# Kernel tuning notes

Hardware: AMD Instinct MI355X
Metric: run time of the kernel (lower is better)

Reference implementation:

```python
import jax, jax.numpy as jnp
import numpy as np

B, N, R, NF, NH = 2, 2048, 16384, 128, 3
PSTEP = 3


def _lin(x, w, b):
    return x @ w + b


def _mlp2(x, w0, b0, w1, b1):
    return jax.nn.relu(_lin(jax.nn.relu(_lin(x, w0, b0)), w1, b1))


def setup_inputs() -> dict:
    key = jax.random.key(0)
    ks = jax.random.split(key, 16)

    def w(k, i, o):
        return (jax.random.normal(k, (i, o), dtype=jnp.float32) / np.float32(np.sqrt(i)))

    a_cur = jax.random.uniform(ks[0], (B, N), dtype=jnp.float32)
    s_cur = jax.random.normal(ks[1], (B, N, 3), dtype=jnp.float32)
    s_delta = jax.random.normal(ks[2], (B, NH, N, 3), dtype=jnp.float32)
    # Rr/Rs: dense one-hot receiver/sender matrices (B, rel_num, N)
    Rr = jax.nn.one_hot(jax.random.randint(ks[3], (B, R), 0, N), N, dtype=jnp.float32)
    Rs = jax.nn.one_hot(jax.random.randint(ks[4], (B, R), 0, N), N, dtype=jnp.float32)
    edge_attrs = (jax.random.uniform(ks[5], (B, R, 1)) > 0.5).astype(jnp.float32)
    z = lambda n: jnp.zeros((n,), dtype=jnp.float32)
    return {
        "a_cur": a_cur, "s_cur": s_cur, "s_delta": s_delta,
        "Rr": Rr, "Rs": Rs, "edge_attrs": edge_attrs,
        "pe_w0": w(ks[6], 3 * NH + 1, NF), "pe_b0": z(NF),
        "pe_w1": w(ks[7], NF, NF), "pe_b1": z(NF),
        "re_w0": w(ks[8], 6, NF), "re_b0": z(NF),
        "re_w1": w(ks[9], NF, NF), "re_b1": z(NF),
        "re_w2": w(ks[10], NF, NF), "re_b2": z(NF),
        "rp_w": w(ks[11], 3 * NF, NF), "rp_b": z(NF),
        "pp_w": w(ks[12], 2 * NF, NF), "pp_b": z(NF),
        "pr_w0": w(ks[13], NF, NF), "pr_b0": z(NF),
        "pr_w1": w(ks[14], NF, 3), "pr_b1": z(3),
    }


def reference(a_cur, s_cur, s_delta, Rr, Rs, edge_attrs,
              pe_w0, pe_b0, pe_w1, pe_b1,
              re_w0, re_b0, re_w1, re_b1, re_w2, re_b2,
              rp_w, rp_b, pp_w, pp_b,
              pr_w0, pr_b0, pr_w1, pr_b1):
    b, nh, n, _ = s_delta.shape
    # (B, n_history, N, 3) -> (B, N, 3*n_history)
    s_delta_flat = jnp.transpose(s_delta, (0, 2, 1, 3)).reshape(b, n, -1)
    a_r = jnp.einsum('brn,bn->br', Rr, a_cur)[..., None]
    a_s = jnp.einsum('brn,bn->br', Rs, a_cur)[..., None]
    s_r = jnp.einsum('brn,bnd->brd', Rr, s_cur)
    s_s = jnp.einsum('brn,bnd->brd', Rs, s_cur)

    particle_encode = _mlp2(jnp.concatenate([s_delta_flat, a_cur[..., None]], -1),
                            pe_w0, pe_b0, pe_w1, pe_b1)
    rel_in = jnp.concatenate([a_r, a_s, s_r - s_s, edge_attrs], -1)
    relation_encode = jax.nn.relu(_lin(
        jax.nn.relu(_lin(jax.nn.relu(_lin(rel_in, re_w0, re_b0)), re_w1, re_b1)),
        re_w2, re_b2))

    effect = particle_encode
    for _ in range(PSTEP):
        e_r = jnp.einsum('brn,bnf->brf', Rr, effect)
        e_s = jnp.einsum('brn,bnf->brf', Rs, effect)
        e_rel = jax.nn.relu(_lin(jnp.concatenate([relation_encode, e_r, e_s], -1), rp_w, rp_b))
        agg = jnp.einsum('brn,brf->bnf', Rr, e_rel)  # Rr^T aggregation
        effect = jax.nn.relu(
            _lin(jnp.concatenate([particle_encode, agg], -1), pp_w, pp_b) + effect)

    pred = _lin(jax.nn.relu(_lin(effect, pr_w0, pr_b0)), pr_w1, pr_b1)
    return pred + s_cur
```

## Files before the change

kernel.cpp:

```cpp
#include <hip/hip_runtime.h>
#include <hip/hip_bf16.h>
#include <stdint.h>

#define B_ 2
#define N_ 2048
#define R_ 16384
#define NF_ 128
#define NH_ 3
#define PSTEP_ 3
#define EDGES (B_ * R_)
#define NODES (B_ * N_)
#define MAXDEG 64
#define PREP_EXB0 1024

typedef _Float16 f16;
typedef _Float16 f16x4 __attribute__((ext_vector_type(4)));
typedef float f32x4 __attribute__((ext_vector_type(4)));

struct GemmLds { f16 Ah[128 * 128], Al[128 * 128], Bh[128 * 128], Bl[128 * 128]; };
struct VecLds {
  float wbuf[64][NF_];
  float xt[NF_][20];
  float ht[NF_][20];
  float w0s[10][NF_];
  float b0s[NF_], b1s[NF_];
  float xs[16][10];
  float w1s[NF_][4];
};
union MainLds { GemmLds g; VecLds v; };

__device__ __forceinline__ void gl16(const f16* g, f16* l) {
  typedef const __attribute__((address_space(1))) uint32_t* gas_t;
  typedef __attribute__((address_space(3))) uint32_t* las_t;
  __builtin_amdgcn_global_load_lds((gas_t)(const void*)g, (las_t)(void*)l, 16, 0, 0);
}

__device__ __forceinline__ void mfma_block(const f16* Ah, const f16* Al,
                                           const f16* Bh, const f16* Bl,
                                           f32x4 (&acc)[8][2], int lane, int w) {
  const int l16 = lane & 15, l4 = lane >> 4;
  #pragma unroll 1
  for (int kk = 0; kk < 8; ++kk) {
    const int c16 = kk * 2 + (l4 >> 1);
    const int sub = (l4 & 1) * 4;
    f16x4 bh[2], bl[2];
    #pragma unroll
    for (int nf = 0; nf < 2; ++nf) {
      const int n = w * 32 + nf * 16 + l16;
      const int off = n * 128 + ((c16 ^ (n & 7)) * 8) + sub;
      bh[nf] = *(const f16x4*)&Bh[off];
      bl[nf] = *(const f16x4*)&Bl[off];
    }
    #pragma unroll
    for (int m = 0; m < 8; ++m) {
      const int r = m * 16 + l16;
      const int off = r * 128 + ((c16 ^ (r & 7)) * 8) + sub;
      const f16x4 ah = *(const f16x4*)&Ah[off];
      const f16x4 al = *(const f16x4*)&Al[off];
      #pragma unroll
      for (int nf = 0; nf < 2; ++nf) {
        acc[m][nf] = __builtin_amdgcn_mfma_f32_16x16x16f16(ah, bh[nf], acc[m][nf], 0, 0, 0);
        acc[m][nf] = __builtin_amdgcn_mfma_f32_16x16x16f16(ah, bl[nf], acc[m][nf], 0, 0, 0);
        acc[m][nf] = __builtin_amdgcn_mfma_f32_16x16x16f16(al, bh[nf], acc[m][nf], 0, 0, 0);
      }
    }
  }
}

__device__ __forceinline__ void frags_to_lds(f32x4 (&acc)[8][2], f16* Ah, f16* Al,
                                             int lane, int w) {
  const int l16 = lane & 15, l4 = lane >> 4;
  #pragma unroll
  for (int m = 0; m < 8; ++m)
    #pragma unroll
    for (int nf = 0; nf < 2; ++nf)
      #pragma unroll
      for (int i = 0; i < 4; ++i) {
        const float v = fmaxf(acc[m][nf][i], 0.f);
        const int row = m * 16 + l4 * 4 + i;
        const int col = w * 32 + nf * 16 + l16;
        const int off = row * 128 + (((col >> 3) ^ (row & 7)) * 8) + (col & 7);
        const f16 h = (f16)v;
        Ah[off] = h; Al[off] = (f16)(v - (float)h);
      }
}

__global__ __launch_bounds__(256) void k_prep(
    const float* __restrict__ Rr, const float* __restrict__ Rs,
    const float* __restrict__ rp_w, const float* __restrict__ re_w1,
    const float* __restrict__ re_w2,
    int* __restrict__ recv, int* __restrict__ send,
    f16* __restrict__ rpT_h, f16* __restrict__ rpT_l,
    f16* __restrict__ re1T_h, f16* __restrict__ re1T_l,
    f16* __restrict__ re2T_h, f16* __restrict__ re2T_l,
    int* __restrict__ counts) {
  const int bid = blockIdx.x, t = threadIdx.x;
  if (bid < 16) {
    counts[bid * 256 + t] = 0;
  } else if (bid < 336) {
    const int i = (bid - 16) * 256 + t;
    const int S1 = 384 * 128, S2 = S1 + 128 * 128, S3 = S2 + 128 * 128;
    if (i < S1) {
      const int k = i >> 7, n = i & 127;
      const float v = rp_w[i];
      const f16 h = (f16)v;
      rpT_h[n * 384 + k] = h; rpT_l[n * 384 + k] = (f16)(v - (float)h);
    } else if (i < S2) {
      const int j = i - S1, k = j >> 7, n = j & 127;
      const float v = re_w1[j];
      const f16 h = (f16)v;
      re1T_h[n * 128 + k] = h; re1T_l[n * 128 + k] = (f16)(v - (float)h);
    } else if (i < S3) {
      const int j = i - S2, k = j >> 7, n = j & 127;
      const float v = re_w2[j];
      const f16 h = (f16)v;
      re2T_h[n * 128 + k] = h; re2T_l[n * 128 + k] = (f16)(v - (float)h);
    }
  } else if (bid >= PREP_EXB0) {
    const int wid = (bid - PREP_EXB0) * 4 + (t >> 6);
    const int lane = t & 63;
    const bool isR = wid < EDGES;
    const int row = isR ? wid : wid - EDGES;
    const float4* p = reinterpret_cast<const float4*>((isR ? Rr : Rs) + (size_t)row * N_);
    int found = 0;
    #pragma unroll 1
    for (int it = 0; it < N_ / 256; ++it) {
      const float4 v = p[it * 64 + lane];
      const int base = (it * 64 + lane) * 4;
      bool hit = false;
      if (v.x != 0.f) { found = base;     hit = true; }
      if (v.y != 0.f) { found = base + 1; hit = true; }
      if (v.z != 0.f) { found = base + 2; hit = true; }
      if (v.w != 0.f) { found = base + 3; hit = true; }
      if (__any(hit)) break;
    }
    #pragma unroll
    for (int off = 32; off > 0; off >>= 1)
      found = max(found, __shfl_down(found, off, 64));
    if (lane == 0) (isR ? recv : send)[row] = found;
  }
}

__global__ __launch_bounds__(256, 1) void k_pre(
    const float* __restrict__ a_cur, const float* __restrict__ s_cur,
    const float* __restrict__ s_delta, const float* __restrict__ ea,
    const int* __restrict__ recv, const int* __restrict__ send,
    const float* __restrict__ pe_w0, const float* __restrict__ pe_b0,
    const float* __restrict__ pe_w1, const float* __restrict__ pe_b1,
    const float* __restrict__ re_w0, const float* __restrict__ re_b0,
    const float* __restrict__ re_b1, const float* __restrict__ re_b2,
    const f16* __restrict__ re1T_h, const f16* __restrict__ re1T_l,
    const f16* __restrict__ re2T_h, const f16* __restrict__ re2T_l,
    float* __restrict__ pe, f16* __restrict__ pe_h, f16* __restrict__ pe_l,
    f16* __restrict__ rel_h, f16* __restrict__ rel_l,
    int* __restrict__ counts, int* __restrict__ bucket) {
  __shared__ MainLds u;
  __shared__ float xt6[6][128];
  __shared__ float w0s6[6][128];
  __shared__ float sb0[128];

  const int bid = blockIdx.x, t = threadIdx.x;
  const int lane = t & 63, w = t >> 6;
  const int l16 = lane & 15, l4 = lane >> 4;
  const int f = t & 127, g = t >> 7;

  {
    const int e = bid * 256 + t;
    if (e < EDGES) {
      const int gnode = (e >> 14) * N_ + recv[e];
      const int pos = atomicAdd(&counts[gnode], 1);
      if (pos < MAXDEG) bucket[gnode * MAXDEG + pos] = e;
    }
  }

  auto stageB = [&](const f16* gh, const f16* gl) {
    #pragma unroll
    for (int rb = 0; rb < 32; rb += 4) {
      const int r0w = w * 32 + rb;
      const int row = r0w + l4;
      const int sc = (l16 ^ (row & 7)) * 8;
      gl16(gh + (size_t)row * 128 + sc, &u.g.Bh[r0w * 128]);
      gl16(gl + (size_t)row * 128 + sc, &u.g.Bl[r0w * 128]);
    }
  };

  {
    const int r0 = bid * 16;
    for (int i = t; i < 10 * NF_; i += 256) u.v.w0s[i >> 7][i & 127] = pe_w0[i];
    if (t < NF_) { u.v.b0s[t] = pe_b0[t]; u.v.b1s[t] = pe_b1[t]; }
    for (int i = t; i < 160; i += 256) {
      const int r = i / 10, k = i % 10;
      const int gr = r0 + r, b = gr >> 11, n = gr & (N_ - 1);
      u.v.xs[r][k] = (k < 9)
          ? s_delta[(((size_t)b * NH_ + (k / 3)) * N_ + n) * 3 + (k % 3)]
          : a_cur[gr];
    }
    __syncthreads();
    for (int r = g * 8; r < g * 8 + 8; ++r) {
      float a1 = u.v.b0s[f];
      #pragma unroll
      for (int k = 0; k < 10; ++k) a1 = fmaf(u.v.xs[r][k], u.v.w0s[k][f], a1);
      u.v.ht[f][r] = fmaxf(a1, 0.f);
    }
    float acc[8];
    #pragma unroll
    for (int i = 0; i < 8; ++i) acc[i] = u.v.b1s[f];
    for (int h = 0; h < 2; ++h) {
      __syncthreads();
      for (int i = t; i < 64 * NF_; i += 256) u.v.wbuf[i >> 7][i & 127] = pe_w1[h * 64 * NF_ + i];
      __syncthreads();
      for (int k = 0; k < 64; ++k) {
        const float wv = u.v.wbuf[k][f];
        #pragma unroll
        for (int i = 0; i < 2; ++i) {
          const float4 x4 = *reinterpret_cast<const float4*>(&u.v.ht[h * 64 + k][g * 8 + i * 4]);
          acc[i*4+0] = fmaf(x4.x, wv, acc[i*4+0]);
          acc[i*4+1] = fmaf(x4.y, wv, acc[i*4+1]);
          acc[i*4+2] = fmaf(x4.z, wv, acc[i*4+2]);
          acc[i*4+3] = fmaf(x4.w, wv, acc[i*4+3]);
        }
      }
    }
    #pragma unroll
    for (int i = 0; i < 8; ++i) {
      const size_t idx = (size_t)(r0 + g * 8 + i) * NF_ + f;
      const float v = fmaxf(acc[i], 0.f);
      pe[idx] = v;
      const f16 h = (f16)v;
      pe_h[idx] = h; pe_l[idx] = (f16)(v - (float)h);
    }
  }
  __syncthreads();

  {
    const int e0 = bid * 128;
    if (t < 128) {
      const int ge = e0 + t, b = ge >> 14;
      const int rc = recv[ge], sd = send[ge];
      xt6[0][t] = a_cur[(b << 11) + rc];
      xt6[1][t] = a_cur[(b << 11) + sd];
      #pragma unroll
      for (int d = 0; d < 3; ++d)
        xt6[2 + d][t] = s_cur[(size_t)((b << 11) + rc) * 3 + d]
                      - s_cur[(size_t)((b << 11) + sd) * 3 + d];
      xt6[5][t] = ea[ge];
    }
    stageB(re1T_h, re1T_l);
    for (int i = t; i < 6 * 128; i += 256) w0s6[i >> 7][i & 127] = re_w0[i];
    if (t < 128) sb0[t] = re_b0[t];
    __syncthreads();
    {
      float wreg[6];
      #pragma unroll
      for (int k = 0; k < 6; ++k) wreg[k] = w0s6[k][f];
      const float b0v = sb0[f];
      for (int r = g * 64; r < g * 64 + 64; ++r) {
        float a1 = b0v;
        #pragma unroll
        for (int k = 0; k < 6; ++k) a1 = fmaf(xt6[k][r], wreg[k], a1);
        a1 = fmaxf(a1, 0.f);
        const int off = r * 128 + ((((f >> 3)) ^ (r & 7)) * 8) + (f & 7);
        const f16 h = (f16)a1;
        u.g.Ah[off] = h; u.g.Al[off] = (f16)(a1 - (float)h);
      }
    }
    __syncthreads();
    f32x4 acc[8][2];
    {
      const float bv0 = re_b1[w * 32 + l16], bv1 = re_b1[w * 32 + 16 + l16];
      #pragma unroll
      for (int m = 0; m < 8; ++m) {
        acc[m][0] = (f32x4){bv0, bv0, bv0, bv0};
        acc[m][1] = (f32x4){bv1, bv1, bv1, bv1};
      }
    }
    mfma_block(u.g.Ah, u.g.Al, u.g.Bh, u.g.Bl, acc, lane, w);
    __syncthreads();
    frags_to_lds(acc, u.g.Ah, u.g.Al, lane, w);
    stageB(re2T_h, re2T_l);
    {
      const float bv0 = re_b2[w * 32 + l16], bv1 = re_b2[w * 32 + 16 + l16];
      #pragma unroll
      for (int m = 0; m < 8; ++m) {
        acc[m][0] = (f32x4){bv0, bv0, bv0, bv0};
        acc[m][1] = (f32x4){bv1, bv1, bv1, bv1};
      }
    }
    __syncthreads();
    mfma_block(u.g.Ah, u.g.Al, u.g.Bh, u.g.Bl, acc, lane, w);
    __syncthreads();
    frags_to_lds(acc, u.g.Ah, u.g.Al, lane, w);
    __syncthreads();
    {
      const int row = t >> 1, hf = t & 1;
      const float4* sA = (const float4*)&u.g.Ah[row * 128 + hf * 64];
      const float4* sL = (const float4*)&u.g.Al[row * 128 + hf * 64];
      float4* dA = (float4*)&rel_h[(size_t)(e0 + row) * 128 + hf * 64];
      float4* dL = (float4*)&rel_l[(size_t)(e0 + row) * 128 + hf * 64];
      #pragma unroll
      for (int j = 0; j < 8; ++j) { dA[j] = sA[j]; dL[j] = sL[j]; }
    }
  }
}

__global__ __launch_bounds__(256, 1) void k_erel(
    const f16* __restrict__ rel_h, const f16* __restrict__ rel_l,
    const f16* __restrict__ src_h, const f16* __restrict__ src_l,
    const int* __restrict__ recv, const int* __restrict__ send,
    const f16* __restrict__ rpT_h, const f16* __restrict__ rpT_l,
    const float* __restrict__ rp_b, float* __restrict__ e_rel) {
  __shared__ GemmLds u;
  __shared__ int eidx0[128], eidx1[128];
  const int bid = blockIdx.x, t = threadIdx.x;
  const int lane = t & 63, w = t >> 6;
  const int l16 = lane & 15, l4 = lane >> 4;
  const int e0 = bid * 128;
  const int b = bid >> 7;
  if (t < 128) eidx0[t] = recv[e0 + t];
  else         eidx1[t - 128] = send[e0 + t - 128];
  f32x4 acc[8][2];
  {
    const float bv0 = rp_b[w * 32 + l16], bv1 = rp_b[w * 32 + 16 + l16];
    #pragma unroll
    for (int m = 0; m < 8; ++m) {
      acc[m][0] = (f32x4){bv0, bv0, bv0, bv0};
      acc[m][1] = (f32x4){bv1, bv1, bv1, bv1};
    }
  }
  #pragma unroll 1
  for (int ch = 0; ch < 3; ++ch) {
    __syncthreads();
    #pragma unroll
    for (int rb = 0; rb < 32; rb += 4) {
      const int r0w = w * 32 + rb;
      const int row = r0w + l4;
      const int ge = e0 + row;
      if (ch == 0) {
        gl16(rel_h + (size_t)ge * 128 + l16 * 8, &u.Ah[r0w * 128]);
        gl16(rel_l + (size_t)ge * 128 + l16 * 8, &u.Al[r0w * 128]);
      } else {
        const int node = (ch == 1) ? eidx0[row] : eidx1[row];
        const size_t ao = ((size_t)(b << 11) + node) * 128 + ((l16 ^ (row & 7)) * 8);
        gl16(src_h + ao, &u.Ah[r0w * 128]);
        gl16(src_l + ao, &u.Al[r0w * 128]);
      }
      const int sc = (l16 ^ (row & 7)) * 8;
      gl16(rpT_h + (size_t)row * 384 + ch * 128 + sc, &u.Bh[r0w * 128]);
      gl16(rpT_l + (size_t)row * 384 + ch * 128 + sc, &u.Bl[r0w * 128]);
    }
    __syncthreads();
    mfma_block(u.Ah, u.Al, u.Bh, u.Bl, acc, lane, w);
  }
  #pragma unroll
  for (int m = 0; m < 8; ++m)
    #pragma unroll
    for (int nf = 0; nf < 2; ++nf)
      #pragma unroll
      for (int i = 0; i < 4; ++i) {
        const float v = fmaxf(acc[m][nf][i], 0.f);
        const int row = e0 + m * 16 + l4 * 4 + i;
        const int col = w * 32 + nf * 16 + l16;
        e_rel[(size_t)row * NF_ + col] = v;
      }
}

__global__ __launch_bounds__(256) void k_update(
    const float* __restrict__ pe, const float* __restrict__ e_rel,
    const int* __restrict__ counts, const int* __restrict__ bucket,
    const float* __restrict__ src_f,
    const float* __restrict__ pp_w, const float* __restrict__ pp_b,
    float* __restrict__ dst_f, f16* __restrict__ dst_h, f16* __restrict__ dst_l,
    const float* __restrict__ s_cur,
    const float* __restrict__ pr_w0, const float* __restrict__ pr_b0,
    const float* __restrict__ pr_w1, const float* __restrict__ pr_b1,
    float* __restrict__ out, int final_step) {
  __shared__ alignas(16) float wbuf[64][NF_];
  __shared__ alignas(16) float xt[NF_][20];
  __shared__ alignas(16) float ht[NF_][20];
  __shared__ float w1s[NF_][4];
  const int t = threadIdx.x, f = t & 127, g = t >> 7;
  const int r0 = blockIdx.x * 16;
  float acc[8];
  {
    const float bias = pp_b[f];
    #pragma unroll
    for (int i = 0; i < 8; ++i) acc[i] = bias;
  }
  for (int c = 0; c < 2; ++c) {
    __syncthreads();
    {
      const int e = t >> 4, k0 = (t & 15) * 8;
      float s[8];
      if (c == 0) {
        const float* srcp = pe + (size_t)(r0 + e) * NF_ + k0;
        const float4 v0 = *reinterpret_cast<const float4*>(srcp);
        const float4 v1 = *reinterpret_cast<const float4*>(srcp + 4);
        s[0]=v0.x; s[1]=v0.y; s[2]=v0.z; s[3]=v0.w;
        s[4]=v1.x; s[5]=v1.y; s[6]=v1.z; s[7]=v1.w;
      } else {
        #pragma unroll
        for (int i = 0; i < 8; ++i) s[i] = 0.f;
        const int gnode = r0 + e;
        const int cnt = min(counts[gnode], MAXDEG);
        for (int i = 0; i < cnt; ++i) {
          const int ed = bucket[gnode * MAXDEG + i];
          const float4 v0 = *reinterpret_cast<const float4*>(&e_rel[(size_t)ed * NF_ + k0]);
          const float4 v1 = *reinterpret_cast<const float4*>(&e_rel[(size_t)ed * NF_ + k0 + 4]);
          s[0]+=v0.x; s[1]+=v0.y; s[2]+=v0.z; s[3]+=v0.w;
          s[4]+=v1.x; s[5]+=v1.y; s[6]+=v1.z; s[7]+=v1.w;
        }
      }
      #pragma unroll
      for (int i = 0; i < 8; ++i) xt[k0 + i][e] = s[i];
    }
    #pragma unroll 1
    for (int h = 0; h < 2; ++h) {
      __syncthreads();
      for (int i = t; i < 64 * NF_; i += 256)
        wbuf[i >> 7][i & 127] = pp_w[(size_t)(c * NF_ + h * 64) * NF_ + i];
      __syncthreads();
      for (int k = 0; k < 64; ++k) {
        const float wv = wbuf[k][f];
        const int ka = h * 64 + k;
        #pragma unroll
        for (int i = 0; i < 2; ++i) {
          const float4 x4 = *reinterpret_cast<const float4*>(&xt[ka][g * 8 + i * 4]);
          acc[i*4+0] = fmaf(x4.x, wv, acc[i*4+0]);
          acc[i*4+1] = fmaf(x4.y, wv, acc[i*4+1]);
          acc[i*4+2] = fmaf(x4.z, wv, acc[i*4+2]);
          acc[i*4+3] = fmaf(x4.w, wv, acc[i*4+3]);
        }
      }
    }
  }
  if (!final_step) {
    #pragma unroll
    for (int i = 0; i < 8; ++i) {
      const size_t idx = (size_t)(r0 + g * 8 + i) * NF_ + f;
      const float v = fmaxf(acc[i] + src_f[idx], 0.f);
      dst_f[idx] = v;
      const f16 h = (f16)v;
      dst_h[idx] = h; dst_l[idx] = (f16)(v - (float)h);
    }
    return;
  }
  __syncthreads();
  #pragma unroll
  for (int i = 0; i < 8; ++i) {
    const size_t idx = (size_t)(r0 + g * 8 + i) * NF_ + f;
    xt[f][g * 8 + i] = fmaxf(acc[i] + src_f[idx], 0.f);
  }
  for (int i = t; i < NF_ * 3; i += 256) w1s[i / 3][i % 3] = pr_w1[i];
  {
    const float bias = pr_b0[f];
    #pragma unroll
    for (int i = 0; i < 8; ++i) acc[i] = bias;
  }
  for (int h = 0; h < 2; ++h) {
    __syncthreads();
    for (int i = t; i < 64 * NF_; i += 256) wbuf[i >> 7][i & 127] = pr_w0[h * 64 * NF_ + i];
    __syncthreads();
    for (int k = 0; k < 64; ++k) {
      const float wv = wbuf[k][f];
      const int ka = h * 64 + k;
      #pragma unroll
      for (int i = 0; i < 2; ++i) {
        const float4 x4 = *reinterpret_cast<const float4*>(&xt[ka][g * 8 + i * 4]);
        acc[i*4+0] = fmaf(x4.x, wv, acc[i*4+0]);
        acc[i*4+1] = fmaf(x4.y, wv, acc[i*4+1]);
        acc[i*4+2] = fmaf(x4.z, wv, acc[i*4+2]);
        acc[i*4+3] = fmaf(x4.w, wv, acc[i*4+3]);
      }
    }
  }
  #pragma unroll
  for (int i = 0; i < 8; ++i) ht[f][g * 8 + i] = fmaxf(acc[i], 0.f);
  __syncthreads();
  if (t < 48) {
    const int r = t / 3, d = t % 3;
    float a2 = pr_b1[d];
    for (int k = 0; k < NF_; ++k) a2 = fmaf(ht[k][r], w1s[k][d], a2);
    const int gr = r0 + r;
    out[(size_t)gr * 3 + d] = a2 + s_cur[(size_t)gr * 3 + d];
  }
}

extern "C" void kernel_launch(void* const* d_in, const int* in_sizes, int n_in,
                              void* d_out, int out_size, void* d_ws, size_t ws_size,
                              hipStream_t stream) {
  (void)in_sizes; (void)n_in; (void)out_size; (void)ws_size;
  const float* a_cur   = (const float*)d_in[0];
  const float* s_cur   = (const float*)d_in[1];
  const float* s_delta = (const float*)d_in[2];
  const float* Rr      = (const float*)d_in[3];
  const float* Rs      = (const float*)d_in[4];
  const float* ea      = (const float*)d_in[5];
  const float* pe_w0 = (const float*)d_in[6];
  const float* pe_b0 = (const float*)d_in[7];
  const float* pe_w1 = (const float*)d_in[8];
  const float* pe_b1 = (const float*)d_in[9];
  const float* re_w0 = (const float*)d_in[10];
  const float* re_b0 = (const float*)d_in[11];
  const float* re_w1 = (const float*)d_in[12];
  const float* re_b1 = (const float*)d_in[13];
  const float* re_w2 = (const float*)d_in[14];
  const float* re_b2 = (const float*)d_in[15];
  const float* rp_w  = (const float*)d_in[16];
  const float* rp_b  = (const float*)d_in[17];
  const float* pp_w  = (const float*)d_in[18];
  const float* pp_b  = (const float*)d_in[19];
  const float* pr_w0 = (const float*)d_in[20];
  const float* pr_b0 = (const float*)d_in[21];
  const float* pr_w1 = (const float*)d_in[22];
  const float* pr_b1 = (const float*)d_in[23];
  float* out = (float*)d_out;

  uint8_t* wp = (uint8_t*)d_ws;
  auto alloc = [&](size_t bytes) {
    void* p = (void*)wp;
    wp += (bytes + 255) & ~(size_t)255;
    return p;
  };
  int* recv   = (int*)alloc(EDGES * 4);
  int* send   = (int*)alloc(EDGES * 4);
  int* counts = (int*)alloc(NODES * 4);
  int* bucket = (int*)alloc((size_t)NODES * MAXDEG * 4);
  float* pe   = (float*)alloc((size_t)NODES * NF_ * 4);
  f16* pe_h   = (f16*)alloc((size_t)NODES * NF_ * 2);
  f16* pe_l   = (f16*)alloc((size_t)NODES * NF_ * 2);
  float* effA = (float*)alloc((size_t)NODES * NF_ * 4);
  f16* effA_h = (f16*)alloc((size_t)NODES * NF_ * 2);
  f16* effA_l = (f16*)alloc((size_t)NODES * NF_ * 2);
  float* effB = (float*)alloc((size_t)NODES * NF_ * 4);
  f16* effB_h = (f16*)alloc((size_t)NODES * NF_ * 2);
  f16* effB_l = (f16*)alloc((size_t)NODES * NF_ * 2);
  float* e_rel = (float*)alloc((size_t)EDGES * NF_ * 4);
  f16* rel_h  = (f16*)alloc((size_t)EDGES * NF_ * 2);
  f16* rel_l  = (f16*)alloc((size_t)EDGES * NF_ * 2);
  f16* rpT_h  = (f16*)alloc(128 * 384 * 2);
  f16* rpT_l  = (f16*)alloc(128 * 384 * 2);
  f16* re1T_h = (f16*)alloc(128 * 128 * 2);
  f16* re1T_l = (f16*)alloc(128 * 128 * 2);
  f16* re2T_h = (f16*)alloc(128 * 128 * 2);
  f16* re2T_l = (f16*)alloc(128 * 128 * 2);

  k_prep<<<PREP_EXB0 + (2 * EDGES) / 4, 256, 0, stream>>>(
      Rr, Rs, rp_w, re_w1, re_w2, recv, send,
      rpT_h, rpT_l, re1T_h, re1T_l, re2T_h, re2T_l, counts);

  k_pre<<<256, 256, 0, stream>>>(
      a_cur, s_cur, s_delta, ea, recv, send,
      pe_w0, pe_b0, pe_w1, pe_b1, re_w0, re_b0, re_b1, re_b2,
      re1T_h, re1T_l, re2T_h, re2T_l,
      pe, pe_h, pe_l, rel_h, rel_l, counts, bucket);

  const float* esrc = pe;
  const f16* esrc_h = pe_h;
  const f16* esrc_l = pe_l;
  for (int s = 0; s < PSTEP_; ++s) {
    float* dst_f = (s == 1) ? effB   : effA;
    f16*  dst_h  = (s == 1) ? effB_h : effA_h;
    f16*  dst_l  = (s == 1) ? effB_l : effA_l;
    k_erel<<<EDGES / 128, 256, 0, stream>>>(rel_h, rel_l, esrc_h, esrc_l,
                                            recv, send, rpT_h, rpT_l, rp_b, e_rel);
    k_update<<<NODES / 16, 256, 0, stream>>>(
        pe, e_rel, counts, bucket, esrc, pp_w, pp_b, dst_f, dst_h, dst_l,
        s_cur, pr_w0, pr_b0, pr_w1, pr_b1, out, (s == PSTEP_ - 1) ? 1 : 0);
    esrc = dst_f; esrc_h = dst_h; esrc_l = dst_l;
  }
}
```

Before: 692.5 us.

## Drop split-f16 hi/lo emulation, use single f16 MFMA and smaller edge tiles

```diff
diff --git a/kernel.cpp b/kernel.cpp
--- a/kernel.cpp
+++ b/kernel.cpp
@@ -17,7 +17,8 @@
 typedef _Float16 f16x4 __attribute__((ext_vector_type(4)));
 typedef float f32x4 __attribute__((ext_vector_type(4)));
 
-struct GemmLds { f16 Ah[128 * 128], Al[128 * 128], Bh[128 * 128], Bl[128 * 128]; };
+struct GemmLds128 { f16 Ah[128 * 128], Bh[128 * 128]; };
+struct GemmLds64  { f16 Ah[64 * 128],  Bh[128 * 128]; };
 struct VecLds {
   float wbuf[64][NF_];
   float xt[NF_][20];
@@ -27,7 +28,7 @@
   float xs[16][10];
   float w1s[NF_][4];
 };
-union MainLds { GemmLds g; VecLds v; };
+union PreLds { GemmLds128 g; VecLds v; };
 
 __device__ __forceinline__ void gl16(const f16* g, f16* l) {
   typedef const __attribute__((address_space(1))) uint32_t* gas_t;
@@ -35,39 +36,32 @@
   __builtin_amdgcn_global_load_lds((gas_t)(const void*)g, (las_t)(void*)l, 16, 0, 0);
 }
 
-__device__ __forceinline__ void mfma_block(const f16* Ah, const f16* Al,
-                                           const f16* Bh, const f16* Bl,
-                                           f32x4 (&acc)[8][2], int lane, int w) {
+template<int MM>
+__device__ __forceinline__ void mfma_blockT(const f16* Ah, const f16* Bh,
+                                            f32x4 (&acc)[MM][2], int lane, int w) {
   const int l16 = lane & 15, l4 = lane >> 4;
   #pragma unroll 1
   for (int kk = 0; kk < 8; ++kk) {
     const int c16 = kk * 2 + (l4 >> 1);
     const int sub = (l4 & 1) * 4;
-    f16x4 bh[2], bl[2];
+    f16x4 bh[2];
     #pragma unroll
     for (int nf = 0; nf < 2; ++nf) {
       const int n = w * 32 + nf * 16 + l16;
-      const int off = n * 128 + ((c16 ^ (n & 7)) * 8) + sub;
-      bh[nf] = *(const f16x4*)&Bh[off];
-      bl[nf] = *(const f16x4*)&Bl[off];
-    }
-    #pragma unroll
-    for (int m = 0; m < 8; ++m) {
+      bh[nf] = *(const f16x4*)&Bh[n * 128 + ((c16 ^ (n & 7)) * 8) + sub];
+    }
+    #pragma unroll
+    for (int m = 0; m < MM; ++m) {
       const int r = m * 16 + l16;
-      const int off = r * 128 + ((c16 ^ (r & 7)) * 8) + sub;
-      const f16x4 ah = *(const f16x4*)&Ah[off];
-      const f16x4 al = *(const f16x4*)&Al[off];
-      #pragma unroll
-      for (int nf = 0; nf < 2; ++nf) {
+      const f16x4 ah = *(const f16x4*)&Ah[r * 128 + ((c16 ^ (r & 7)) * 8) + sub];
+      #pragma unroll
+      for (int nf = 0; nf < 2; ++nf)
         acc[m][nf] = __builtin_amdgcn_mfma_f32_16x16x16f16(ah, bh[nf], acc[m][nf], 0, 0, 0);
-        acc[m][nf] = __builtin_amdgcn_mfma_f32_16x16x16f16(ah, bl[nf], acc[m][nf], 0, 0, 0);
-        acc[m][nf] = __builtin_amdgcn_mfma_f32_16x16x16f16(al, bh[nf], acc[m][nf], 0, 0, 0);
-      }
-    }
-  }
-}
-
-__device__ __forceinline__ void frags_to_lds(f32x4 (&acc)[8][2], f16* Ah, f16* Al,
+    }
+  }
+}
+
+__device__ __forceinline__ void frags_to_lds(f32x4 (&acc)[8][2], f16* Ah,
                                              int lane, int w) {
   const int l16 = lane & 15, l4 = lane >> 4;
   #pragma unroll
@@ -79,9 +73,7 @@
         const float v = fmaxf(acc[m][nf][i], 0.f);
         const int row = m * 16 + l4 * 4 + i;
         const int col = w * 32 + nf * 16 + l16;
-        const int off = row * 128 + (((col >> 3) ^ (row & 7)) * 8) + (col & 7);
-        const f16 h = (f16)v;
-        Ah[off] = h; Al[off] = (f16)(v - (float)h);
+        Ah[row * 128 + (((col >> 3) ^ (row & 7)) * 8) + (col & 7)] = (f16)v;
       }
 }
 
@@ -90,9 +82,7 @@
     const float* __restrict__ rp_w, const float* __restrict__ re_w1,
     const float* __restrict__ re_w2,
     int* __restrict__ recv, int* __restrict__ send,
-    f16* __restrict__ rpT_h, f16* __restrict__ rpT_l,
-    f16* __restrict__ re1T_h, f16* __restrict__ re1T_l,
-    f16* __restrict__ re2T_h, f16* __restrict__ re2T_l,
+    f16* __restrict__ rpT_h, f16* __restrict__ re1T_h, f16* __restrict__ re2T_h,
     int* __restrict__ counts) {
   const int bid = blockIdx.x, t = threadIdx.x;
   if (bid < 16) {
@@ -102,19 +92,13 @@
     const int S1 = 384 * 128, S2 = S1 + 128 * 128, S3 = S2 + 128 * 128;
     if (i < S1) {
       const int k = i >> 7, n = i & 127;
-      const float v = rp_w[i];
-      const f16 h = (f16)v;
-      rpT_h[n * 384 + k] = h; rpT_l[n * 384 + k] = (f16)(v - (float)h);
+      rpT_h[n * 384 + k] = (f16)rp_w[i];
     } else if (i < S2) {
       const int j = i - S1, k = j >> 7, n = j & 127;
-      const float v = re_w1[j];
-      const f16 h = (f16)v;
-      re1T_h[n * 128 + k] = h; re1T_l[n * 128 + k] = (f16)(v - (float)h);
+      re1T_h[n * 128 + k] = (f16)re_w1[j];
     } else if (i < S3) {
       const int j = i - S2, k = j >> 7, n = j & 127;
-      const float v = re_w2[j];
-      const f16 h = (f16)v;
-      re2T_h[n * 128 + k] = h; re2T_l[n * 128 + k] = (f16)(v - (float)h);
+      re2T_h[n * 128 + k] = (f16)re_w2[j];
     }
   } else if (bid >= PREP_EXB0) {
     const int wid = (bid - PREP_EXB0) * 4 + (t >> 6);
@@ -141,7 +125,7 @@
   }
 }
 
-__global__ __launch_bounds__(256, 1) void k_pre(
+__global__ __launch_bounds__(256, 2) void k_pre(
     const float* __restrict__ a_cur, const float* __restrict__ s_cur,
     const float* __restrict__ s_delta, const float* __restrict__ ea,
     const int* __restrict__ recv, const int* __restrict__ send,
@@ -149,12 +133,11 @@
     const float* __restrict__ pe_w1, const float* __restrict__ pe_b1,
     const float* __restrict__ re_w0, const float* __restrict__ re_b0,
     const float* __restrict__ re_b1, const float* __restrict__ re_b2,
-    const f16* __restrict__ re1T_h, const f16* __restrict__ re1T_l,
-    const f16* __restrict__ re2T_h, const f16* __restrict__ re2T_l,
-    float* __restrict__ pe, f16* __restrict__ pe_h, f16* __restrict__ pe_l,
-    f16* __restrict__ rel_h, f16* __restrict__ rel_l,
+    const f16* __restrict__ re1T_h, const f16* __restrict__ re2T_h,
+    float* __restrict__ pe, f16* __restrict__ pe_h,
+    f16* __restrict__ rel_h,
     int* __restrict__ counts, int* __restrict__ bucket) {
-  __shared__ MainLds u;
+  __shared__ PreLds u;
   __shared__ float xt6[6][128];
   __shared__ float w0s6[6][128];
   __shared__ float sb0[128];
@@ -164,6 +147,9 @@
   const int l16 = lane & 15, l4 = lane >> 4;
   const int f = t & 127, g = t >> 7;
 
+  {
+    const int e = bid * 128 + t;
+  }
   {
     const int e = bid * 256 + t;
     if (e < EDGES) {
@@ -173,14 +159,13 @@
     }
   }
 
-  auto stageB = [&](const f16* gh, const f16* gl) {
+  auto stageB = [&](const f16* gh) {
     #pragma unroll
     for (int rb = 0; rb < 32; rb += 4) {
       const int r0w = w * 32 + rb;
       const int row = r0w + l4;
       const int sc = (l16 ^ (row & 7)) * 8;
       gl16(gh + (size_t)row * 128 + sc, &u.g.Bh[r0w * 128]);
-      gl16(gl + (size_t)row * 128 + sc, &u.g.Bl[r0w * 128]);
     }
   };
 
@@ -190,9 +175,9 @@
     if (t < NF_) { u.v.b0s[t] = pe_b0[t]; u.v.b1s[t] = pe_b1[t]; }
     for (int i = t; i < 160; i += 256) {
       const int r = i / 10, k = i % 10;
-      const int gr = r0 + r, b = gr >> 11, n = gr & (N_ - 1);
+      const int gr = r0 + r, bb = gr >> 11, n = gr & (N_ - 1);
       u.v.xs[r][k] = (k < 9)
-          ? s_delta[(((size_t)b * NH_ + (k / 3)) * N_ + n) * 3 + (k % 3)]
+          ? s_delta[(((size_t)bb * NH_ + (k / 3)) * N_ + n) * 3 + (k % 3)]
           : a_cur[gr];
     }
     __syncthreads();
@@ -226,8 +211,7 @@
       const size_t idx = (size_t)(r0 + g * 8 + i) * NF_ + f;
       const float v = fmaxf(acc[i], 0.f);
       pe[idx] = v;
-      const f16 h = (f16)v;
-      pe_h[idx] = h; pe_l[idx] = (f16)(v - (float)h);
+      pe_h[idx] = (f16)v;
     }
   }
   __syncthreads();
@@ -235,17 +219,17 @@
   {
     const int e0 = bid * 128;
     if (t < 128) {
-      const int ge = e0 + t, b = ge >> 14;
+      const int ge = e0 + t, bb = ge >> 14;
       const int rc = recv[ge], sd = send[ge];
-      xt6[0][t] = a_cur[(b << 11) + rc];
-      xt6[1][t] = a_cur[(b << 11) + sd];
+      xt6[0][t] = a_cur[(bb << 11) + rc];
+      xt6[1][t] = a_cur[(bb << 11) + sd];
       #pragma unroll
       for (int d = 0; d < 3; ++d)
-        xt6[2 + d][t] = s_cur[(size_t)((b << 11) + rc) * 3 + d]
-                      - s_cur[(size_t)((b << 11) + sd) * 3 + d];
+        xt6[2 + d][t] = s_cur[(size_t)((bb << 11) + rc) * 3 + d]
+                      - s_cur[(size_t)((bb << 11) + sd) * 3 + d];
       xt6[5][t] = ea[ge];
     }
-    stageB(re1T_h, re1T_l);
+    stageB(re1T_h);
     for (int i = t; i < 6 * 128; i += 256) w0s6[i >> 7][i & 127] = re_w0[i];
     if (t < 128) sb0[t] = re_b0[t];
     __syncthreads();
@@ -259,9 +243,7 @@
         #pragma unroll
         for (int k = 0; k < 6; ++k) a1 = fmaf(xt6[k][r], wreg[k], a1);
         a1 = fmaxf(a1, 0.f);
-        const int off = r * 128 + ((((f >> 3)) ^ (r & 7)) * 8) + (f & 7);
-        const f16 h = (f16)a1;
-        u.g.Ah[off] = h; u.g.Al[off] = (f16)(a1 - (float)h);
+        u.g.Ah[r * 128 + ((((f >> 3)) ^ (r & 7)) * 8) + (f & 7)] = (f16)a1;
       }
     }
     __syncthreads();
@@ -274,10 +256,10 @@
         acc[m][1] = (f32x4){bv1, bv1, bv1, bv1};
       }
     }
-    mfma_block(u.g.Ah, u.g.Al, u.g.Bh, u.g.Bl, acc, lane, w);
-    __syncthreads();
-    frags_to_lds(acc, u.g.Ah, u.g.Al, lane, w);
-    stageB(re2T_h, re2T_l);
+    mfma_blockT<8>(u.g.Ah, u.g.Bh, acc, lane, w);
+    __syncthreads();
+    frags_to_lds(acc, u.g.Ah, lane, w);
+    stageB(re2T_h);
     {
       const float bv0 = re_b2[w * 32 + l16], bv1 = re_b2[w * 32 + 16 + l16];
       #pragma unroll
@@ -287,42 +269,39 @@
       }
     }
     __syncthreads();
-    mfma_block(u.g.Ah, u.g.Al, u.g.Bh, u.g.Bl, acc, lane, w);
-    __syncthreads();
-    frags_to_lds(acc, u.g.Ah, u.g.Al, lane, w);
+    mfma_blockT<8>(u.g.Ah, u.g.Bh, acc, lane, w);
+    __syncthreads();
+    frags_to_lds(acc, u.g.Ah, lane, w);
     __syncthreads();
     {
       const int row = t >> 1, hf = t & 1;
       const float4* sA = (const float4*)&u.g.Ah[row * 128 + hf * 64];
-      const float4* sL = (const float4*)&u.g.Al[row * 128 + hf * 64];
       float4* dA = (float4*)&rel_h[(size_t)(e0 + row) * 128 + hf * 64];
-      float4* dL = (float4*)&rel_l[(size_t)(e0 + row) * 128 + hf * 64];
-      #pragma unroll
-      for (int j = 0; j < 8; ++j) { dA[j] = sA[j]; dL[j] = sL[j]; }
-    }
-  }
-}
-
-__global__ __launch_bounds__(256, 1) void k_erel(
-    const f16* __restrict__ rel_h, const f16* __restrict__ rel_l,
-    const f16* __restrict__ src_h, const f16* __restrict__ src_l,
+      #pragma unroll
+      for (int j = 0; j < 8; ++j) dA[j] = sA[j];
+    }
+  }
+}
+
+__global__ __launch_bounds__(256, 2) void k_erel(
+    const f16* __restrict__ rel_h, const f16* __restrict__ src_h,
     const int* __restrict__ recv, const int* __restrict__ send,
-    const f16* __restrict__ rpT_h, const f16* __restrict__ rpT_l,
+    const f16* __restrict__ rpT_h,
     const float* __restrict__ rp_b, float* __restrict__ e_rel) {
-  __shared__ GemmLds u;
-  __shared__ int eidx0[128], eidx1[128];
+  __shared__ GemmLds64 u;
+  __shared__ int eidx0[64], eidx1[64];
   const int bid = blockIdx.x, t = threadIdx.x;
   const int lane = t & 63, w = t >> 6;
   const int l16 = lane & 15, l4 = lane >> 4;
-  const int e0 = bid * 128;
-  const int b = bid >> 7;
-  if (t < 128) eidx0[t] = recv[e0 + t];
-  else         eidx1[t - 128] = send[e0 + t - 128];
-  f32x4 acc[8][2];
+  const int e0 = bid * 64;
+  const int b = bid >> 8;
+  if (t < 64) eidx0[t] = recv[e0 + t];
+  else if (t < 128) eidx1[t - 64] = send[e0 + t - 64];
+  f32x4 acc[4][2];
   {
     const float bv0 = rp_b[w * 32 + l16], bv1 = rp_b[w * 32 + 16 + l16];
     #pragma unroll
-    for (int m = 0; m < 8; ++m) {
+    for (int m = 0; m < 4; ++m) {
       acc[m][0] = (f32x4){bv0, bv0, bv0, bv0};
       acc[m][1] = (f32x4){bv1, bv1, bv1, bv1};
     }
@@ -331,28 +310,30 @@
   for (int ch = 0; ch < 3; ++ch) {
     __syncthreads();
     #pragma unroll
-    for (int rb = 0; rb < 32; rb += 4) {
-      const int r0w = w * 32 + rb;
+    for (int rb = 0; rb < 16; rb += 4) {
+      const int r0w = w * 16 + rb;
       const int row = r0w + l4;
       const int ge = e0 + row;
       if (ch == 0) {
         gl16(rel_h + (size_t)ge * 128 + l16 * 8, &u.Ah[r0w * 128]);
-        gl16(rel_l + (size_t)ge * 128 + l16 * 8, &u.Al[r0w * 128]);
       } else {
         const int node = (ch == 1) ? eidx0[row] : eidx1[row];
         const size_t ao = ((size_t)(b << 11) + node) * 128 + ((l16 ^ (row & 7)) * 8);
         gl16(src_h + ao, &u.Ah[r0w * 128]);
-        gl16(src_l + ao, &u.Al[r0w * 128]);
-      }
+      }
+    }
+    #pragma unroll
+    for (int rb = 0; rb < 32; rb += 4) {
+      const int r0w = w * 32 + rb;
+      const int row = r0w + l4;
       const int sc = (l16 ^ (row & 7)) * 8;
       gl16(rpT_h + (size_t)row * 384 + ch * 128 + sc, &u.Bh[r0w * 128]);
-      gl16(rpT_l + (size_t)row * 384 + ch * 128 + sc, &u.Bl[r0w * 128]);
-    }
-    __syncthreads();
-    mfma_block(u.Ah, u.Al, u.Bh, u.Bl, acc, lane, w);
+    }
+    __syncthreads();
+    mfma_blockT<4>(u.Ah, u.Bh, acc, lane, w);
   }
   #pragma unroll
-  for (int m = 0; m < 8; ++m)
+  for (int m = 0; m < 4; ++m)
     #pragma unroll
     for (int nf = 0; nf < 2; ++nf)
       #pragma unroll
@@ -364,12 +345,12 @@
       }
 }
 
-__global__ __launch_bounds__(256) void k_update(
+__global__ __launch_bounds__(256, 2) void k_update(
     const float* __restrict__ pe, const float* __restrict__ e_rel,
     const int* __restrict__ counts, const int* __restrict__ bucket,
     const float* __restrict__ src_f,
     const float* __restrict__ pp_w, const float* __restrict__ pp_b,
-    float* __restrict__ dst_f, f16* __restrict__ dst_h, f16* __restrict__ dst_l,
+    float* __restrict__ dst_f, f16* __restrict__ dst_h,
     const float* __restrict__ s_cur,
     const float* __restrict__ pr_w0, const float* __restrict__ pr_b0,
     const float* __restrict__ pr_w1, const float* __restrict__ pr_b1,
@@ -439,8 +420,7 @@
       const size_t idx = (size_t)(r0 + g * 8 + i) * NF_ + f;
       const float v = fmaxf(acc[i] + src_f[idx], 0.f);
       dst_f[idx] = v;
-      const f16 h = (f16)v;
-      dst_h[idx] = h; dst_l[idx] = (f16)(v - (float)h);
+      dst_h[idx] = (f16)v;
     }
     return;
   }
@@ -527,45 +507,35 @@
   int* bucket = (int*)alloc((size_t)NODES * MAXDEG * 4);
   float* pe   = (float*)alloc((size_t)NODES * NF_ * 4);
   f16* pe_h   = (f16*)alloc((size_t)NODES * NF_ * 2);
-  f16* pe_l   = (f16*)alloc((size_t)NODES * NF_ * 2);
   float* effA = (float*)alloc((size_t)NODES * NF_ * 4);
   f16* effA_h = (f16*)alloc((size_t)NODES * NF_ * 2);
-  f16* effA_l = (f16*)alloc((size_t)NODES * NF_ * 2);
   float* effB = (float*)alloc((size_t)NODES * NF_ * 4);
   f16* effB_h = (f16*)alloc((size_t)NODES * NF_ * 2);
-  f16* effB_l = (f16*)alloc((size_t)NODES * NF_ * 2);
   float* e_rel = (float*)alloc((size_t)EDGES * NF_ * 4);
   f16* rel_h  = (f16*)alloc((size_t)EDGES * NF_ * 2);
-  f16* rel_l  = (f16*)alloc((size_t)EDGES * NF_ * 2);
   f16* rpT_h  = (f16*)alloc(128 * 384 * 2);
-  f16* rpT_l  = (f16*)alloc(128 * 384 * 2);
   f16* re1T_h = (f16*)alloc(128 * 128 * 2);
-  f16* re1T_l = (f16*)alloc(128 * 128 * 2);
   f16* re2T_h = (f16*)alloc(128 * 128 * 2);
-  f16* re2T_l = (f16*)alloc(128 * 128 * 2);
 
   k_prep<<<PREP_EXB0 + (2 * EDGES) / 4, 256, 0, stream>>>(
       Rr, Rs, rp_w, re_w1, re_w2, recv, send,
-      rpT_h, rpT_l, re1T_h, re1T_l, re2T_h, re2T_l, counts);
+      rpT_h, re1T_h, re2T_h, counts);
 
   k_pre<<<256, 256, 0, stream>>>(
       a_cur, s_cur, s_delta, ea, recv, send,
       pe_w0, pe_b0, pe_w1, pe_b1, re_w0, re_b0, re_b1, re_b2,
-      re1T_h, re1T_l, re2T_h, re2T_l,
-      pe, pe_h, pe_l, rel_h, rel_l, counts, bucket);
+      re1T_h, re2T_h, pe, pe_h, rel_h, counts, bucket);
 
   const float* esrc = pe;
   const f16* esrc_h = pe_h;
-  const f16* esrc_l = pe_l;
   for (int s = 0; s < PSTEP_; ++s) {
     float* dst_f = (s == 1) ? effB   : effA;
     f16*  dst_h  = (s == 1) ? effB_h : effA_h;
-    f16*  dst_l  = (s == 1) ? effB_l : effA_l;
-    k_erel<<<EDGES / 128, 256, 0, stream>>>(rel_h, rel_l, esrc_h, esrc_l,
-                                            recv, send, rpT_h, rpT_l, rp_b, e_rel);
+    k_erel<<<EDGES / 64, 256, 0, stream>>>(rel_h, esrc_h, recv, send,
+                                           rpT_h, rp_b, e_rel);
     k_update<<<NODES / 16, 256, 0, stream>>>(
-        pe, e_rel, counts, bucket, esrc, pp_w, pp_b, dst_f, dst_h, dst_l,
+        pe, e_rel, counts, bucket, esrc, pp_w, pp_b, dst_f, dst_h,
         s_cur, pr_w0, pr_b0, pr_w1, pr_b1, out, (s == PSTEP_ - 1) ? 1 : 0);
-    esrc = dst_f; esrc_h = dst_h; esrc_l = dst_l;
-  }
-}
+    esrc = dst_f; esrc_h = dst_h;
+  }
+}
```

New measurement: 661.2 us. 4.5% less time.
